# Kernel optimization log

Measured on AMD Instinct MI355X. Metric: run time of the kernel, lower is better.

The kernel has to match this reference:

```python
import jax, jax.numpy as jnp
import numpy as np

B, N, P = 8192, 4096, 8
D = N // P  # 512
EPS = 1e-5


def setup_inputs() -> dict:
    key = jax.random.key(0)
    ks = jax.random.split(key, 7)
    bound = 1.0 / np.sqrt(D)
    return {
        "x": jax.random.normal(ks[0], (B, N), dtype=jnp.float32),
        "weights1": jax.random.normal(ks[1], (P, D, D), dtype=jnp.float32) * bound,
        "bias1": jax.random.uniform(ks[2], (N,), jnp.float32, -bound, bound),
        "weights2": jax.random.normal(ks[3], (P, D, D), dtype=jnp.float32) * bound,
        "bias2": jax.random.uniform(ks[4], (N,), jnp.float32, -bound, bound),
        "bn_weight": jnp.ones((N,), jnp.float32),
        "bn_bias": jnp.zeros((N,), jnp.float32),
        "gamma3": jax.random.normal(ks[5], (N,), jnp.float32) * 0.1,
        "beta3": jax.random.normal(ks[6], (N,), jnp.float32) * 0.1,
    }


def _block_matmul(x, w):
    # x: [B, N], w: [P, D, D] -> equivalent to x @ block_diag(*w)
    b = x.shape[0]
    return jnp.einsum("bpd,pde->bpe", x.reshape(b, P, D), w).reshape(b, N)


def reference(x, weights1, bias1, weights2, bias2, bn_weight, bn_bias, gamma3, beta3):
    h = _block_matmul(x, weights1) + bias1  # [B, N]
    # BatchNorm1d in training mode: biased batch statistics over the batch axis
    mean = jnp.mean(h, axis=0)
    var = jnp.mean((h - mean) ** 2, axis=0)
    o1 = (h - mean) * jax.lax.rsqrt(var + EPS) * bn_weight + bn_bias
    o3 = _block_matmul(o1, weights2) + bias2 + x  # residual
    # sigmoid-gated activation: (gamma + sigmoid(beta*x)*(1-gamma)) * x
    o4 = (gamma3 + jax.nn.sigmoid(beta3 * o3) * (1.0 - gamma3)) * o3
    return o4
```

## Files before the change

### kernel.cpp

```cpp
#include <hip/hip_runtime.h>
#include <hip/hip_bf16.h>
#include <cstdint>
#include <cstddef>

#define B_ROWS 8192
#define N_COLS 4096
#define P_BLK 8
#define D_BLK 512
#define EPSV 1e-5f

typedef __bf16 bf16x8 __attribute__((ext_vector_type(8)));
typedef float f32x4 __attribute__((ext_vector_type(4)));

__device__ __forceinline__ void async_ld16(const void* g, void* l) {
    __builtin_amdgcn_global_load_lds(
        (const __attribute__((address_space(1))) void*)g,
        (__attribute__((address_space(3))) void*)l,
        16, 0, 0);
}

__global__ __launch_bounds__(256) void cvt_x_k(const float* __restrict__ x,
                                               __hip_bfloat16* __restrict__ xb) {
    size_t i = ((size_t)blockIdx.x * 256 + threadIdx.x) * 8;
    float4 v0 = *(const float4*)(x + i);
    float4 v1 = *(const float4*)(x + i + 4);
    union { __hip_bfloat16 h[8]; uint4 u; } r;
    r.h[0] = __float2bfloat16(v0.x); r.h[1] = __float2bfloat16(v0.y);
    r.h[2] = __float2bfloat16(v0.z); r.h[3] = __float2bfloat16(v0.w);
    r.h[4] = __float2bfloat16(v1.x); r.h[5] = __float2bfloat16(v1.y);
    r.h[6] = __float2bfloat16(v1.z); r.h[7] = __float2bfloat16(v1.w);
    *(uint4*)(xb + i) = r.u;
}

__global__ __launch_bounds__(256) void tr_w_k(const float* __restrict__ W,
                                              const float* __restrict__ scale,
                                              __hip_bfloat16* __restrict__ Wt) {
    __shared__ float t[32][33];
    int p = blockIdx.z;
    int d0 = blockIdx.x * 32, e0 = blockIdx.y * 32;
    const float* Wp = W + (size_t)p * D_BLK * D_BLK;
    for (int j = 0; j < 32; j += 8) {
        int d = d0 + threadIdx.y + j;
        float v = Wp[(size_t)d * D_BLK + e0 + threadIdx.x];
        if (scale) v *= scale[p * D_BLK + d];
        t[threadIdx.y + j][threadIdx.x] = v;
    }
    __syncthreads();
    __hip_bfloat16* Wtp = Wt + (size_t)p * D_BLK * D_BLK;
    for (int j = 0; j < 32; j += 8) {
        int e = e0 + threadIdx.y + j;
        Wtp[(size_t)e * D_BLK + d0 + threadIdx.x] =
            __float2bfloat16(t[threadIdx.x][threadIdx.y + j]);
    }
}

__global__ __launch_bounds__(256) void finalize_k(const float* __restrict__ sum,
                                                  const float* __restrict__ sumsq,
                                                  const float* __restrict__ bnw,
                                                  const float* __restrict__ bnb,
                                                  float* __restrict__ a,
                                                  float* __restrict__ c) {
    int i = blockIdx.x * 256 + threadIdx.x;
    float m = sum[i] * (1.0f / B_ROWS);
    float var = sumsq[i] * (1.0f / B_ROWS) - m * m;
    float ai = bnw[i] * rsqrtf(var + EPSV);
    a[i] = ai;
    c[i] = bnb[i] - m * ai;
}

__global__ __launch_bounds__(256) void bias2p_k(const float* __restrict__ W2,
                                                const float* __restrict__ c,
                                                const float* __restrict__ bias2,
                                                float* __restrict__ out) {
    int col = blockIdx.x * 256 + threadIdx.x;
    int p = col >> 9;
    int e = col & (D_BLK - 1);
    const float* Wp = W2 + (size_t)p * D_BLK * D_BLK + e;
    const float* cp = c + p * D_BLK;
    float acc = 0.0f;
    for (int d = 0; d < D_BLK; d++) acc += cp[d] * Wp[(size_t)d * D_BLK];
    out[col] = bias2[col] + acc;
}

__device__ __forceinline__ void gemm_core(const __hip_bfloat16* __restrict__ A,
                                          const __hip_bfloat16* __restrict__ Bt,
                                          f32x4 acc[4][4]) {
    __shared__ __hip_bfloat16 As[128 * 32];
    __shared__ __hip_bfloat16 Bs[128 * 32];

    const int tid = threadIdx.x;
    const int lane = tid & 63;
    const int wave = tid >> 6;
    const int wm = (wave >> 1) * 64;
    const int wn = (wave & 1) * 64;
    const int row_base = blockIdx.x * 128;
    const int col_base = blockIdx.y * 128;
    const int p = col_base >> 9;
    const int ebase = col_base & (D_BLK - 1);

    const int ar = tid >> 2;
    const int kp = (tid & 3) * 8;
    const __hip_bfloat16* a_src0 = A + (size_t)(row_base + ar) * N_COLS + p * D_BLK + kp;
    const __hip_bfloat16* a_src1 = a_src0 + (size_t)64 * N_COLS;
    const __hip_bfloat16* b_src0 = Bt + (size_t)(p * D_BLK + ebase + ar) * D_BLK + kp;
    const __hip_bfloat16* b_src1 = b_src0 + (size_t)64 * D_BLK;
    __hip_bfloat16* a_dst0 = &As[ar * 32 + kp];
    __hip_bfloat16* a_dst1 = &As[(ar + 64) * 32 + kp];
    __hip_bfloat16* b_dst0 = &Bs[ar * 32 + kp];
    __hip_bfloat16* b_dst1 = &Bs[(ar + 64) * 32 + kp];

    const int fm = lane & 15;
    const int fkoff = (lane >> 4) * 8;

    for (int i = 0; i < 4; i++)
        for (int j = 0; j < 4; j++)
            acc[i][j] = (f32x4){0.0f, 0.0f, 0.0f, 0.0f};

    for (int k0 = 0; k0 < D_BLK; k0 += 32) {
        async_ld16(a_src0, a_dst0);
        async_ld16(a_src1, a_dst1);
        async_ld16(b_src0, b_dst0);
        async_ld16(b_src1, b_dst1);
        a_src0 += 32; a_src1 += 32; b_src0 += 32; b_src1 += 32;
        __syncthreads();

        bf16x8 af[4], bfr[4];
#pragma unroll
        for (int i = 0; i < 4; i++)
            af[i] = *(const bf16x8*)&As[(wm + i * 16 + fm) * 32 + fkoff];
#pragma unroll
        for (int j = 0; j < 4; j++)
            bfr[j] = *(const bf16x8*)&Bs[(wn + j * 16 + fm) * 32 + fkoff];
#pragma unroll
        for (int i = 0; i < 4; i++)
#pragma unroll
            for (int j = 0; j < 4; j++)
                acc[i][j] = __builtin_amdgcn_mfma_f32_16x16x32_bf16(
                    af[i], bfr[j], acc[i][j], 0, 0, 0);
        __syncthreads();
    }
}

__global__ __launch_bounds__(256) void gemm1_k(const __hip_bfloat16* __restrict__ xb,
                                               const __hip_bfloat16* __restrict__ w1t,
                                               const float* __restrict__ bias1,
                                               __hip_bfloat16* __restrict__ h,
                                               float* __restrict__ sum,
                                               float* __restrict__ sumsq) {
    f32x4 acc[4][4];
    gemm_core(xb, w1t, acc);

    const int tid = threadIdx.x;
    const int lane = tid & 63;
    const int wave = tid >> 6;
    const int wm = (wave >> 1) * 64;
    const int wn = (wave & 1) * 64;
    const int row_base = blockIdx.x * 128;
    const int col_base = blockIdx.y * 128;
    const int cr = (lane >> 4) * 4;
    const int cc = lane & 15;

#pragma unroll
    for (int j = 0; j < 4; j++) {
        const int col = col_base + wn + j * 16 + cc;
        const float b1 = bias1[col];
        float s = 0.0f, sq = 0.0f;
#pragma unroll
        for (int i = 0; i < 4; i++) {
            const int row0 = row_base + wm + i * 16 + cr;
#pragma unroll
            for (int r = 0; r < 4; r++) {
                float v = acc[i][j][r] + b1;
                h[(size_t)(row0 + r) * N_COLS + col] = __float2bfloat16(v);
                s += v;
                sq += v * v;
            }
        }
        s  += __shfl_xor(s, 16);  s  += __shfl_xor(s, 32);
        sq += __shfl_xor(sq, 16); sq += __shfl_xor(sq, 32);
        if (lane < 16) {
            atomicAdd(&sum[col], s);
            atomicAdd(&sumsq[col], sq);
        }
    }
}

__global__ __launch_bounds__(256) void gemm2_k(const __hip_bfloat16* __restrict__ h,
                                               const __hip_bfloat16* __restrict__ w2t,
                                               const float* __restrict__ bias2p,
                                               const float* __restrict__ x,
                                               const float* __restrict__ gamma3,
                                               const float* __restrict__ beta3,
                                               float* __restrict__ out) {
    f32x4 acc[4][4];
    gemm_core(h, w2t, acc);

    const int tid = threadIdx.x;
    const int lane = tid & 63;
    const int wave = tid >> 6;
    const int wm = (wave >> 1) * 64;
    const int wn = (wave & 1) * 64;
    const int row_base = blockIdx.x * 128;
    const int col_base = blockIdx.y * 128;
    const int cr = (lane >> 4) * 4;
    const int cc = lane & 15;

#pragma unroll
    for (int j = 0; j < 4; j++) {
        const int col = col_base + wn + j * 16 + cc;
        const float bb = bias2p[col];
        const float g  = gamma3[col];
        const float be = beta3[col];
#pragma unroll
        for (int i = 0; i < 4; i++) {
            const int row0 = row_base + wm + i * 16 + cr;
#pragma unroll
            for (int r = 0; r < 4; r++) {
                const size_t idx = (size_t)(row0 + r) * N_COLS + col;
                float o3 = acc[i][j][r] + bb + x[idx];
                float sg = 1.0f / (1.0f + expf(-be * o3));
                out[idx] = (g + sg * (1.0f - g)) * o3;
            }
        }
    }
}

extern "C" void kernel_launch(void* const* d_in, const int* in_sizes, int n_in,
                              void* d_out, int out_size, void* d_ws, size_t ws_size,
                              hipStream_t stream) {
    const float* x     = (const float*)d_in[0];
    const float* W1    = (const float*)d_in[1];
    const float* bias1 = (const float*)d_in[2];
    const float* W2    = (const float*)d_in[3];
    const float* bias2 = (const float*)d_in[4];
    const float* bnw   = (const float*)d_in[5];
    const float* bnb   = (const float*)d_in[6];
    const float* gam3  = (const float*)d_in[7];
    const float* bet3  = (const float*)d_in[8];
    float* out = (float*)d_out;

    char* ws = (char*)d_ws;
    const size_t XB_BYTES = (size_t)B_ROWS * N_COLS * 2;
    const size_t H_BYTES  = (size_t)B_ROWS * N_COLS * 2;
    const size_t WT_BYTES = (size_t)P_BLK * D_BLK * D_BLK * 2;
    const size_t V_BYTES  = (size_t)N_COLS * 4;

    __hip_bfloat16* xb   = (__hip_bfloat16*)(ws);
    __hip_bfloat16* hbuf = (__hip_bfloat16*)(ws + XB_BYTES);
    __hip_bfloat16* w1t  = (__hip_bfloat16*)(ws + XB_BYTES + H_BYTES);
    __hip_bfloat16* w2t  = (__hip_bfloat16*)(ws + XB_BYTES + H_BYTES + WT_BYTES);
    float* sums  = (float*)(ws + XB_BYTES + H_BYTES + 2 * WT_BYTES);
    float* sumsq = (float*)((char*)sums + V_BYTES);
    float* a_sc  = (float*)((char*)sums + 2 * V_BYTES);
    float* c_sh  = (float*)((char*)sums + 3 * V_BYTES);
    float* b2p   = (float*)((char*)sums + 4 * V_BYTES);

    (void)in_sizes; (void)n_in; (void)out_size; (void)ws_size;

    hipMemsetAsync(sums, 0, 2 * V_BYTES, stream);

    cvt_x_k<<<dim3((B_ROWS * N_COLS) / (256 * 8)), dim3(256), 0, stream>>>(x, xb);
    tr_w_k<<<dim3(16, 16, 8), dim3(32, 8), 0, stream>>>(W1, nullptr, w1t);
    gemm1_k<<<dim3(B_ROWS / 128, N_COLS / 128), dim3(256), 0, stream>>>(
        xb, w1t, bias1, hbuf, sums, sumsq);
    finalize_k<<<dim3(N_COLS / 256), dim3(256), 0, stream>>>(sums, sumsq, bnw, bnb, a_sc, c_sh);
    tr_w_k<<<dim3(16, 16, 8), dim3(32, 8), 0, stream>>>(W2, a_sc, w2t);
    bias2p_k<<<dim3(N_COLS / 256), dim3(256), 0, stream>>>(W2, c_sh, bias2, b2p);
    gemm2_k<<<dim3(B_ROWS / 128, N_COLS / 128), dim3(256), 0, stream>>>(
        hbuf, w2t, b2p, x, gam3, bet3, out);
}
```

Measured before the change: 463.9 us.

## Double-buffer GEMM LDS tiles, swizzle layout, and read bf16 residual

The shared GEMM core now keeps two LDS buffers, so the async global-to-LDS load of the next k-tile is issued while the current tile feeds the MFMAs. This also removes one barrier per iteration. LDS rows are XOR-swizzled to cut bank conflicts on fragment reads, and both GEMMs get an occupancy hint in launch_bounds. The gemm2 epilogue reads the residual from the bf16 copy of x instead of fp32, halving that traffic at the cost of precision in the residual term.

```diff
diff --git a/kernel.cpp b/kernel.cpp
--- a/kernel.cpp
+++ b/kernel.cpp
@@ -85,8 +85,8 @@
 __device__ __forceinline__ void gemm_core(const __hip_bfloat16* __restrict__ A,
                                           const __hip_bfloat16* __restrict__ Bt,
                                           f32x4 acc[4][4]) {
-    __shared__ __hip_bfloat16 As[128 * 32];
-    __shared__ __hip_bfloat16 Bs[128 * 32];
+    __shared__ __hip_bfloat16 As[2][128 * 32];
+    __shared__ __hip_bfloat16 Bs[2][128 * 32];
 
     const int tid = threadIdx.x;
     const int lane = tid & 63;
@@ -99,54 +99,62 @@
     const int ebase = col_base & (D_BLK - 1);
 
     const int ar = tid >> 2;
-    const int kp = (tid & 3) * 8;
-    const __hip_bfloat16* a_src0 = A + (size_t)(row_base + ar) * N_COLS + p * D_BLK + kp;
+    const int c4 = tid & 3;
+    const int kq8 = (c4 ^ ((tid >> 3) & 3)) * 8;
+    const int dst_off = ar * 32 + c4 * 8;
+
+    const __hip_bfloat16* a_src0 = A + (size_t)(row_base + ar) * N_COLS + p * D_BLK + kq8;
     const __hip_bfloat16* a_src1 = a_src0 + (size_t)64 * N_COLS;
-    const __hip_bfloat16* b_src0 = Bt + (size_t)(p * D_BLK + ebase + ar) * D_BLK + kp;
+    const __hip_bfloat16* b_src0 = Bt + (size_t)(p * D_BLK + ebase + ar) * D_BLK + kq8;
     const __hip_bfloat16* b_src1 = b_src0 + (size_t)64 * D_BLK;
-    __hip_bfloat16* a_dst0 = &As[ar * 32 + kp];
-    __hip_bfloat16* a_dst1 = &As[(ar + 64) * 32 + kp];
-    __hip_bfloat16* b_dst0 = &Bs[ar * 32 + kp];
-    __hip_bfloat16* b_dst1 = &Bs[(ar + 64) * 32 + kp];
 
     const int fm = lane & 15;
-    const int fkoff = (lane >> 4) * 8;
+    const int fkoff = ((lane >> 4) ^ ((fm >> 1) & 3)) * 8;
 
     for (int i = 0; i < 4; i++)
         for (int j = 0; j < 4; j++)
             acc[i][j] = (f32x4){0.0f, 0.0f, 0.0f, 0.0f};
 
-    for (int k0 = 0; k0 < D_BLK; k0 += 32) {
-        async_ld16(a_src0, a_dst0);
-        async_ld16(a_src1, a_dst1);
-        async_ld16(b_src0, b_dst0);
-        async_ld16(b_src1, b_dst1);
-        a_src0 += 32; a_src1 += 32; b_src0 += 32; b_src1 += 32;
+    async_ld16(a_src0, &As[0][dst_off]);
+    async_ld16(a_src1, &As[0][dst_off + 64 * 32]);
+    async_ld16(b_src0, &Bs[0][dst_off]);
+    async_ld16(b_src1, &Bs[0][dst_off + 64 * 32]);
+    a_src0 += 32; a_src1 += 32; b_src0 += 32; b_src1 += 32;
+
+    for (int k = 0; k < 16; k++) {
+        const int cur = k & 1;
         __syncthreads();
+        if (k < 15) {
+            const int nxt = 1 - cur;
+            async_ld16(a_src0, &As[nxt][dst_off]);
+            async_ld16(a_src1, &As[nxt][dst_off + 64 * 32]);
+            async_ld16(b_src0, &Bs[nxt][dst_off]);
+            async_ld16(b_src1, &Bs[nxt][dst_off + 64 * 32]);
+            a_src0 += 32; a_src1 += 32; b_src0 += 32; b_src1 += 32;
+        }
 
         bf16x8 af[4], bfr[4];
 #pragma unroll
         for (int i = 0; i < 4; i++)
-            af[i] = *(const bf16x8*)&As[(wm + i * 16 + fm) * 32 + fkoff];
+            af[i] = *(const bf16x8*)&As[cur][(wm + i * 16 + fm) * 32 + fkoff];
 #pragma unroll
         for (int j = 0; j < 4; j++)
-            bfr[j] = *(const bf16x8*)&Bs[(wn + j * 16 + fm) * 32 + fkoff];
+            bfr[j] = *(const bf16x8*)&Bs[cur][(wn + j * 16 + fm) * 32 + fkoff];
 #pragma unroll
         for (int i = 0; i < 4; i++)
 #pragma unroll
             for (int j = 0; j < 4; j++)
                 acc[i][j] = __builtin_amdgcn_mfma_f32_16x16x32_bf16(
                     af[i], bfr[j], acc[i][j], 0, 0, 0);
-        __syncthreads();
-    }
-}
-
-__global__ __launch_bounds__(256) void gemm1_k(const __hip_bfloat16* __restrict__ xb,
-                                               const __hip_bfloat16* __restrict__ w1t,
-                                               const float* __restrict__ bias1,
-                                               __hip_bfloat16* __restrict__ h,
-                                               float* __restrict__ sum,
-                                               float* __restrict__ sumsq) {
+    }
+}
+
+__global__ __launch_bounds__(256, 4) void gemm1_k(const __hip_bfloat16* __restrict__ xb,
+                                                  const __hip_bfloat16* __restrict__ w1t,
+                                                  const float* __restrict__ bias1,
+                                                  __hip_bfloat16* __restrict__ h,
+                                                  float* __restrict__ sum,
+                                                  float* __restrict__ sumsq) {
     f32x4 acc[4][4];
     gemm_core(xb, w1t, acc);
 
@@ -185,13 +193,13 @@
     }
 }
 
-__global__ __launch_bounds__(256) void gemm2_k(const __hip_bfloat16* __restrict__ h,
-                                               const __hip_bfloat16* __restrict__ w2t,
-                                               const float* __restrict__ bias2p,
-                                               const float* __restrict__ x,
-                                               const float* __restrict__ gamma3,
-                                               const float* __restrict__ beta3,
-                                               float* __restrict__ out) {
+__global__ __launch_bounds__(256, 4) void gemm2_k(const __hip_bfloat16* __restrict__ h,
+                                                  const __hip_bfloat16* __restrict__ w2t,
+                                                  const float* __restrict__ bias2p,
+                                                  const __hip_bfloat16* __restrict__ xb,
+                                                  const float* __restrict__ gamma3,
+                                                  const float* __restrict__ beta3,
+                                                  float* __restrict__ out) {
     f32x4 acc[4][4];
     gemm_core(h, w2t, acc);
 
@@ -217,7 +225,7 @@
 #pragma unroll
             for (int r = 0; r < 4; r++) {
                 const size_t idx = (size_t)(row0 + r) * N_COLS + col;
-                float o3 = acc[i][j][r] + bb + x[idx];
+                float o3 = acc[i][j][r] + bb + __bfloat162float(xb[idx]);
                 float sg = 1.0f / (1.0f + expf(-be * o3));
                 out[idx] = (g + sg * (1.0f - g)) * o3;
             }
@@ -267,5 +275,5 @@
     tr_w_k<<<dim3(16, 16, 8), dim3(32, 8), 0, stream>>>(W2, a_sc, w2t);
     bias2p_k<<<dim3(N_COLS / 256), dim3(256), 0, stream>>>(W2, c_sh, bias2, b2p);
     gemm2_k<<<dim3(B_ROWS / 128, N_COLS / 128), dim3(256), 0, stream>>>(
-        hbuf, w2t, b2p, x, gam3, bet3, out);
-}
+        hbuf, w2t, b2p, xb, gam3, bet3, out);
+}
```

Result: slower. 493.5 us (+6.4%).
